# Optimization experiments

Measured on AMD Instinct MI355X. Metric: run time of the kernel, lower is better.

Reference implementation:

```python
import jax, jax.numpy as jnp
import numpy as np

# Model dims (match init_kwargs)
B_, L, D_MODEL = 1, 2048, 1024
D_INNER, D_CONV, DT_RANK, D_STATE = 2048, 4, 64, 16


def setup_inputs() -> dict:
    key = jax.random.key(0)
    ks = jax.random.split(key, 8)
    s = lambda k, shape, scale: jax.random.normal(k, shape, jnp.float32) * scale
    return {
        "x": jax.random.normal(ks[0], (B_, L, D_MODEL), jnp.float32),
        "in_proj_w": s(ks[1], (D_MODEL, 2 * D_INNER), 0.02),
        "in_proj_b": jnp.zeros((2 * D_INNER,), jnp.float32),
        "conv_w": s(ks[2], (D_CONV, D_INNER), 0.1),          # depthwise kernel, one tap-vector per channel
        "conv_b": jnp.zeros((D_INNER,), jnp.float32),
        "x_proj_w": s(ks[3], (D_INNER, DT_RANK + 2 * D_STATE), 0.02),
        "dt_proj_w": s(ks[4], (DT_RANK, D_INNER), 0.1),
        "dt_proj_b": s(ks[5], (D_INNER,), 0.1),
        "A_log": jnp.log(jnp.tile(jnp.arange(1, D_STATE + 1, dtype=jnp.float32), (D_INNER, 1))),  # S4D-real init
        "D": jnp.ones((D_INNER,), jnp.float32),
        "out_proj_w": s(ks[6], (D_INNER, D_MODEL), 0.02),
        "out_proj_b": jnp.zeros((D_MODEL,), jnp.float32),
    }


def _mamba_forward(x, in_proj_w, in_proj_b, conv_w, conv_b, x_proj_w,
                   dt_proj_w, dt_proj_b, A_log, D, out_proj_w, out_proj_b):
    b, l, _ = x.shape
    d_inner = conv_w.shape[1]
    d_state = A_log.shape[1]

    # in_proj -> split into ssm path and gating residual
    x_and_res = x @ in_proj_w + in_proj_b                 # [b, l, 2*d_inner]
    xin, res = jnp.split(x_and_res, 2, axis=-1)

    # causal depthwise conv1d over the sequence dim (pad left d_conv-1, trunc to l)
    xp = jnp.pad(xin, ((0, 0), (D_CONV - 1, 0), (0, 0)))
    kern = conv_w[:, None, :]                             # [W, I=1, O=d_inner]
    xc = jax.lax.conv_general_dilated(
        xp, kern, window_strides=(1,), padding="VALID",
        dimension_numbers=("NWC", "WIO", "NWC"),
        feature_group_count=d_inner) + conv_b             # [b, l, d_inner]
    u = jax.nn.silu(xc)

    # selective SSM: input-dependent dt, B, C
    A = -jnp.exp(A_log)                                   # [d_inner, d_state]
    dbc = u @ x_proj_w                                    # [b, l, dt_rank + 2*d_state]
    dt, Bm, Cm = jnp.split(dbc, [DT_RANK, DT_RANK + d_state], axis=-1)
    delta = jax.nn.softplus(dt @ dt_proj_w + dt_proj_b)   # [b, l, d_inner]

    deltaA = jnp.exp(jnp.einsum("bld,dn->bldn", delta, A))          # [b, l, d_inner, d_state]
    deltaBu = jnp.einsum("bld,bln,bld->bldn", delta, Bm, u)         # [b, l, d_inner, d_state]

    def step(h, inp):
        dA_t, dBu_t, C_t = inp
        h = dA_t * h + dBu_t                              # [b, d_inner, d_state]
        y_t = jnp.einsum("bdn,bn->bd", h, C_t)
        return h, y_t

    h0 = jnp.zeros((b, d_inner, d_state), u.dtype)
    _, ys = jax.lax.scan(
        step, h0,
        (deltaA.transpose(1, 0, 2, 3), deltaBu.transpose(1, 0, 2, 3), Cm.transpose(1, 0, 2)))
    y = ys.transpose(1, 0, 2) + u * D                     # skip connection via D

    # gate and out-project
    y = y * jax.nn.silu(res)
    return y @ out_proj_w + out_proj_b                    # [b, l, d_model]


def reference(x, in_proj_w, in_proj_b, conv_w, conv_b, x_proj_w,
              dt_proj_w, dt_proj_b, A_log, D, out_proj_w, out_proj_b):
    return _mamba_forward(x, in_proj_w, in_proj_b, conv_w, conv_b, x_proj_w,
                          dt_proj_w, dt_proj_b, A_log, D, out_proj_w, out_proj_b)
```

## Files before the change

kernel.cpp:

```cpp
#include <hip/hip_runtime.h>


#define L_SEQ 2048
#define DMODEL 1024
#define DINNER 2048
#define NSTATE 16
#define DTRANK 64
#define NPROJ_PAD 128

typedef __attribute__((ext_vector_type(8))) short short8;
typedef __attribute__((ext_vector_type(4))) float f32x4;

__device__ __forceinline__ unsigned short f2bf(float f) {
  unsigned int u = __float_as_uint(f);
  u += 0x7FFFu + ((u >> 16) & 1u);
  return (unsigned short)(u >> 16);
}

__device__ __forceinline__ void gload16(const void* g, void* l) {
  __builtin_amdgcn_global_load_lds((const __attribute__((address_space(1))) void*)g,
                                   (__attribute__((address_space(3))) void*)l, 16, 0, 0);
}

__global__ void prep_kernel(const float* __restrict__ in_proj_w, const float* __restrict__ x_proj_w,
                            const float* __restrict__ dt_proj_w,
                            const float* __restrict__ out_proj_w, const float* __restrict__ x,
                            unsigned short* __restrict__ w1t, unsigned short* __restrict__ w3t,
                            unsigned short* __restrict__ w4t, unsigned short* __restrict__ w5t,
                            unsigned short* __restrict__ xb) {
  const int bx = blockIdx.x;
  const int tx = threadIdx.x, ty = threadIdx.y;
  const int id = ty * 32 + tx;

  if (bx >= 6464) {
    if (bx < 8512) {
      const int fid = (bx - 6464) * 256 + id;
      f32x4 v = ((const f32x4*)x)[fid];
      ushort4 o;
      o.x = f2bf(v.x); o.y = f2bf(v.y); o.z = f2bf(v.z); o.w = f2bf(v.w);
      ((ushort4*)xb)[fid] = o;
    } else {
      const int fid = (bx - 8512) * 256 + id;
      ((uint4*)(w3t + 96 * 2048))[fid] = (uint4){0, 0, 0, 0};
    }
    return;
  }

  const float* in;
  unsigned short* out;
  int R, C, rel, gx;
  if (bx < 4096) { in = in_proj_w; out = w1t; R = 1024; C = 4096; rel = bx; gx = 128; }
  else if (bx < 4288) { in = x_proj_w; out = w3t; R = 2048; C = 96; rel = bx - 4096; gx = 3; }
  else if (bx < 4416) { in = dt_proj_w; out = w4t; R = 64; C = 2048; rel = bx - 4288; gx = 64; }
  else { in = out_proj_w; out = w5t; R = 2048; C = 1024; rel = bx - 4416; gx = 32; }
  const int c0 = (rel % gx) * 32, r0 = (rel / gx) * 32;

  __shared__ float tile[32][33];
  for (int y = ty; y < 32; y += 8) tile[y][tx] = in[(size_t)(r0 + y) * C + c0 + tx];
  __syncthreads();
  for (int y = ty; y < 32; y += 8) out[(size_t)(c0 + y) * R + r0 + tx] = f2bf(tile[tx][y]);
}

__global__ void conv_silu_kernel(const float* __restrict__ xres, const float* __restrict__ cw,
                                 const float* __restrict__ cb, float* __restrict__ u,
                                 unsigned short* __restrict__ ub) {
  const int id = blockIdx.x * 256 + threadIdx.x;
  const int t = id >> 11;
  const int d = id & (DINNER - 1);
  float acc = cb[d];
#pragma unroll
  for (int j = 0; j < 4; j++) {
    int tt = t - 3 + j;
    if (tt >= 0) acc += xres[(size_t)tt * (2 * DINNER) + d] * cw[j * DINNER + d];
  }
  float s = acc / (1.f + __expf(-acc));
  u[id] = s;
  ub[id] = f2bf(s);
}

template <int EPI>
__global__ void gemm_bf16(const unsigned short* __restrict__ A,
                          const unsigned short* __restrict__ Bt, float* __restrict__ C,
                          const float* __restrict__ bias, int M, int N, int K, int KS) {
  __shared__ __align__(16) unsigned short lA[2][128 * 64];
  __shared__ __align__(16) unsigned short lB[2][128 * 64];
  const int tid = threadIdx.x;
  const int w = tid >> 6;
  const int lane = tid & 63;
  const int m0 = blockIdx.x * 128;
  const int n0 = blockIdx.y * 128;
  const int kbase = blockIdx.z * KS;
  const int lr = lane >> 3;
  const int srcoff = ((lane & 7) ^ lr) * 8;
  const int wm = (w & 1) * 64;
  const int wn = (w >> 1) * 64;
  const int ml = lane & 15;
  const int quad = lane >> 4;

  f32x4 acc[4][4];
#pragma unroll
  for (int i = 0; i < 4; i++)
#pragma unroll
    for (int j = 0; j < 4; j++) acc[i][j] = (f32x4){0.f, 0.f, 0.f, 0.f};

  const unsigned short* Ag = A + (size_t)m0 * K + kbase;
  const unsigned short* Bg = Bt + (size_t)n0 * K + kbase;

  const int niter = KS >> 6;
  auto stage = [&](int buf, int kk) {
#pragma unroll
    for (int c2 = 0; c2 < 4; c2++) {
      const int row = w * 32 + c2 * 8 + lr;
      gload16(Ag + (size_t)row * K + kk + srcoff, &lA[buf][(w * 32 + c2 * 8) * 64]);
      gload16(Bg + (size_t)row * K + kk + srcoff, &lB[buf][(w * 32 + c2 * 8) * 64]);
    }
  };

  stage(0, 0);
  for (int it = 0; it < niter; it++) {
    __syncthreads();
    if (it + 1 < niter) stage((it + 1) & 1, (it + 1) << 6);
    const unsigned short* bufA = lA[it & 1];
    const unsigned short* bufB = lB[it & 1];
#pragma unroll
    for (int ks = 0; ks < 2; ks++) {
      short8 af[4], bfr[4];
#pragma unroll
      for (int i = 0; i < 4; i++) {
        const int row = wm + i * 16 + ml;
        const int q = ((ks * 4 + quad) ^ (ml & 7)) * 8;
        af[i] = *(const short8*)&bufA[row * 64 + q];
      }
#pragma unroll
      for (int j = 0; j < 4; j++) {
        const int row = wn + j * 16 + ml;
        const int q = ((ks * 4 + quad) ^ (ml & 7)) * 8;
        bfr[j] = *(const short8*)&bufB[row * 64 + q];
      }
#pragma unroll
      for (int i = 0; i < 4; i++)
#pragma unroll
        for (int j = 0; j < 4; j++)
          acc[i][j] = __builtin_amdgcn_mfma_f32_16x16x32_bf16(af[i], bfr[j], acc[i][j], 0, 0, 0);
    }
  }

  float* Cp = (EPI == 3) ? C + (size_t)blockIdx.z * M * N : C;
#pragma unroll
  for (int i = 0; i < 4; i++) {
#pragma unroll
    for (int j = 0; j < 4; j++) {
      const int col = n0 + wn + j * 16 + ml;
      float bv = 0.f;
      if ((EPI == 0 || EPI == 1) && bias != nullptr) bv = bias[col];
#pragma unroll
      for (int r = 0; r < 4; r++) {
        const int row = m0 + wm + i * 16 + quad * 4 + r;
        float v = acc[i][j][r];
        if (EPI == 2) {
          atomicAdd(&Cp[(size_t)row * N + col], v);
        } else {
          v += bv;
          if (EPI == 1) v = (v > 15.f) ? v : __logf(1.f + __expf(v));
          Cp[(size_t)row * N + col] = v;
        }
      }
    }
  }
}

__global__ void reduce_dbc_kernel(const float* __restrict__ part, float* __restrict__ dbc,
                                  unsigned short* __restrict__ dtb) {
  const int id = blockIdx.x * 256 + threadIdx.x;
  float s = 0.f;
#pragma unroll
  for (int z = 0; z < 16; z++) s += part[(size_t)z * (L_SEQ * NPROJ_PAD) + id];
  dbc[id] = s;
  const int col = id & 127;
  if (col < 64) dtb[(id >> 7) * 64 + col] = f2bf(s);
}

__global__ void reduce_out_kernel(const float* __restrict__ part, const float* __restrict__ bias,
                                  float* __restrict__ out) {
  const int fid = blockIdx.x * 256 + threadIdx.x;
  const f32x4* p = (const f32x4*)part;
  const int stride = (L_SEQ * DMODEL) / 4;
  f32x4 v = p[fid];
  v += p[fid + stride];
  v += p[fid + 2 * stride];
  v += p[fid + 3 * stride];
  v += ((const f32x4*)bias)[fid & 255];
  ((f32x4*)out)[fid] = v;
}

__global__ void bias_init_kernel(float* __restrict__ out, const float* __restrict__ b, int nmask) {
  int id = blockIdx.x * 256 + threadIdx.x;
  out[id] = b[id & nmask];
}
__global__ void cast_dt_kernel(const float* __restrict__ dbc, unsigned short* __restrict__ dtb) {
  int id = blockIdx.x * 256 + threadIdx.x;
  int t = id >> 6, k = id & 63;
  dtb[id] = f2bf(dbc[t * NPROJ_PAD + k]);
}


template <int TCH_T>
__global__ void scan1_kernel(const float* __restrict__ delta, const float* __restrict__ u,
                             const float* __restrict__ dbc, const float* __restrict__ A_log,
                             float* __restrict__ P, float* __restrict__ Hz) {
  __shared__ float Bs[TCH_T][NSTATE];
  const int d = blockIdx.x * 256 + threadIdx.x;
  const int c = blockIdx.y;
  for (int idx = threadIdx.x; idx < TCH_T * NSTATE; idx += 256) {
    int t = idx >> 4, n = idx & 15;
    Bs[t][n] = dbc[(size_t)(c * TCH_T + t) * NPROJ_PAD + DTRANK + n];
  }
  float Ad[16], h[16], p[16];
#pragma unroll
  for (int n = 0; n < 16; n++) {
    Ad[n] = -__expf(A_log[d * 16 + n]);
    h[n] = 0.f;
    p[n] = 1.f;
  }
  __syncthreads();
#pragma unroll
  for (int t = 0; t < TCH_T; t++) {
    const int tt = c * TCH_T + t;
    float dl = delta[(size_t)tt * DINNER + d];
    float uu = u[(size_t)tt * DINNER + d];
    float du = dl * uu;
#pragma unroll
    for (int n = 0; n < 16; n++) {
      float dA = __expf(dl * Ad[n]);
      p[n] *= dA;
      h[n] = dA * h[n] + du * Bs[t][n];
    }
  }
#pragma unroll
  for (int n = 0; n < 16; n++) {
    P[(size_t)(c * 16 + n) * DINNER + d] = p[n];
    Hz[(size_t)(c * 16 + n) * DINNER + d] = h[n];
  }
}

__global__ void scan_carry_kernel(const float* __restrict__ P, const float* __restrict__ Hz,
                                  float* __restrict__ H0, int nchunk) {
  const int id = blockIdx.x * 256 + threadIdx.x;
  float h = 0.f;
#pragma unroll 8
  for (int c = 0; c < nchunk; c++) {
    H0[c * (NSTATE * DINNER) + id] = h;
    h = P[c * (NSTATE * DINNER) + id] * h + Hz[c * (NSTATE * DINNER) + id];
  }
}

template <int TCH_T>
__global__ void scan2_kernel(const float* __restrict__ delta, const float* __restrict__ u,
                             const float* __restrict__ dbc, const float* __restrict__ A_log,
                             const float* __restrict__ Dv, const float* __restrict__ xres,
                             const float* __restrict__ H0, unsigned short* __restrict__ ygb) {
  __shared__ float Bs[TCH_T][NSTATE];
  __shared__ float Cs[TCH_T][NSTATE];
  const int d = blockIdx.x * 256 + threadIdx.x;
  const int c = blockIdx.y;
  for (int idx = threadIdx.x; idx < TCH_T * 2 * NSTATE; idx += 256) {
    int t = idx >> 5, q = idx & 31;
    float v = dbc[(size_t)(c * TCH_T + t) * NPROJ_PAD + DTRANK + q];
    if (q < 16) Bs[t][q] = v;
    else Cs[t][q - 16] = v;
  }
  float Ad[16], h[16];
#pragma unroll
  for (int n = 0; n < 16; n++) {
    Ad[n] = -__expf(A_log[d * 16 + n]);
    h[n] = H0[(size_t)(c * 16 + n) * DINNER + d];
  }
  const float Dd = Dv[d];
  __syncthreads();
#pragma unroll
  for (int t = 0; t < TCH_T; t++) {
    const int tt = c * TCH_T + t;
    float dl = delta[(size_t)tt * DINNER + d];
    float uu = u[(size_t)tt * DINNER + d];
    float r = xres[(size_t)tt * (2 * DINNER) + DINNER + d];
    float du = dl * uu;
    float y0 = 0.f, y1 = 0.f;
#pragma unroll
    for (int n = 0; n < 16; n++) {
      float dA = __expf(dl * Ad[n]);
      h[n] = dA * h[n] + du * Bs[t][n];
      if (n & 1) y1 += h[n] * Cs[t][n];
      else y0 += h[n] * Cs[t][n];
    }
    float sil = r / (1.f + __expf(-r));
    float yg = (y0 + y1 + uu * Dd) * sil;
    ygb[(size_t)tt * DINNER + d] = f2bf(yg);
  }
}


extern "C" void kernel_launch(void* const* d_in, const int* in_sizes, int n_in, void* d_out,
                              int out_size, void* d_ws, size_t ws_size, hipStream_t stream) {
  const float* x = (const float*)d_in[0];
  const float* in_proj_w = (const float*)d_in[1];
  const float* in_proj_b = (const float*)d_in[2];
  const float* conv_w = (const float*)d_in[3];
  const float* conv_b = (const float*)d_in[4];
  const float* x_proj_w = (const float*)d_in[5];
  const float* dt_proj_w = (const float*)d_in[6];
  const float* dt_proj_b = (const float*)d_in[7];
  const float* A_log = (const float*)d_in[8];
  const float* Dvec = (const float*)d_in[9];
  const float* out_proj_w = (const float*)d_in[10];
  const float* out_proj_b = (const float*)d_in[11];
  float* out = (float*)d_out;
  char* ws = (char*)d_ws;

  const size_t MB = 1048576;
  const size_t XB = 0;
  const size_t W1T = 4 * MB;
  const size_t XRES = 12 * MB;
  const size_t U = 44 * MB;
  const size_t UB = 60 * MB;
  const size_t W3T = 68 * MB;
  const size_t DBC = W3T + 524288;
  const size_t DTB = DBC + MB;
  const size_t W4T = DTB + 262144;
  const size_t DELTA = 70 * MB;
  const size_t YGB = 86 * MB;
  const size_t W5T = 94 * MB;
  const size_t PBUF = 98 * MB;
  (void)in_sizes; (void)n_in; (void)out_size;

  const bool big = ws_size >= PBUF + 3 * (size_t)(128 * NSTATE * DINNER) * 4;
  prep_kernel<<<8544, dim3(32, 8), 0, stream>>>(
      in_proj_w, x_proj_w, dt_proj_w, out_proj_w, x, (unsigned short*)(ws + W1T),
      (unsigned short*)(ws + W3T), (unsigned short*)(ws + W4T), (unsigned short*)(ws + W5T),
      (unsigned short*)(ws + XB));

  gemm_bf16<0><<<dim3(16, 32, 1), 256, 0, stream>>>(
      (const unsigned short*)(ws + XB), (const unsigned short*)(ws + W1T), (float*)(ws + XRES),
      in_proj_b, 2048, 4096, 1024, 1024);

  conv_silu_kernel<<<(L_SEQ * DINNER) / 256, 256, 0, stream>>>(
      (const float*)(ws + XRES), conv_w, conv_b, (float*)(ws + U), (unsigned short*)(ws + UB));

  if (big) {
    const int tch = 16, nch = 128;
    const size_t PB = (size_t)nch * NSTATE * DINNER * 4;
    const size_t HZB = PBUF + PB;
    const size_t H0B = PBUF + 2 * PB;
    const size_t G3P = PBUF;
    const size_t G2P = PBUF;

    gemm_bf16<3><<<dim3(16, 1, 16), 256, 0, stream>>>(
        (const unsigned short*)(ws + UB), (const unsigned short*)(ws + W3T), (float*)(ws + G3P),
        nullptr, 2048, NPROJ_PAD, 2048, 128);
    reduce_dbc_kernel<<<(L_SEQ * NPROJ_PAD) / 256, 256, 0, stream>>>(
        (const float*)(ws + G3P), (float*)(ws + DBC), (unsigned short*)(ws + DTB));

    gemm_bf16<1><<<dim3(16, 16, 1), 256, 0, stream>>>(
        (const unsigned short*)(ws + DTB), (const unsigned short*)(ws + W4T), (float*)(ws + DELTA),
        dt_proj_b, 2048, 2048, 64, 64);

    const dim3 sgrid(DINNER / 256, nch);
    scan1_kernel<16><<<sgrid, 256, 0, stream>>>(
        (const float*)(ws + DELTA), (const float*)(ws + U), (const float*)(ws + DBC), A_log,
        (float*)(ws + PBUF), (float*)(ws + HZB));
    scan_carry_kernel<<<(NSTATE * DINNER) / 256, 256, 0, stream>>>(
        (const float*)(ws + PBUF), (const float*)(ws + HZB), (float*)(ws + H0B), nch);
    scan2_kernel<16><<<sgrid, 256, 0, stream>>>(
        (const float*)(ws + DELTA), (const float*)(ws + U), (const float*)(ws + DBC), A_log, Dvec,
        (const float*)(ws + XRES), (const float*)(ws + H0B), (unsigned short*)(ws + YGB));

    gemm_bf16<3><<<dim3(16, 8, 4), 256, 0, stream>>>(
        (const unsigned short*)(ws + YGB), (const unsigned short*)(ws + W5T), (float*)(ws + G2P),
        nullptr, 2048, 1024, 2048, 512);
    reduce_out_kernel<<<(L_SEQ * DMODEL) / 1024, 256, 0, stream>>>((const float*)(ws + G2P),
                                                                   out_proj_b, out);
    (void)tch;
  } else {
    hipMemsetAsync(ws + DBC, 0, (size_t)L_SEQ * NPROJ_PAD * 4, stream);
    gemm_bf16<2><<<dim3(16, 1, 16), 256, 0, stream>>>(
        (const unsigned short*)(ws + UB), (const unsigned short*)(ws + W3T), (float*)(ws + DBC),
        nullptr, 2048, NPROJ_PAD, 2048, 128);
    cast_dt_kernel<<<(L_SEQ * DTRANK) / 256, 256, 0, stream>>>((const float*)(ws + DBC),
                                                               (unsigned short*)(ws + DTB));
    gemm_bf16<1><<<dim3(16, 16, 1), 256, 0, stream>>>(
        (const unsigned short*)(ws + DTB), (const unsigned short*)(ws + W4T), (float*)(ws + DELTA),
        dt_proj_b, 2048, 2048, 64, 64);
    const int tch = 64, nch = 32;
    const size_t PB = (size_t)nch * NSTATE * DINNER * 4;
    const size_t HZB = PBUF + PB;
    const size_t H0B = PBUF + 2 * PB;
    const dim3 sgrid(DINNER / 256, nch);
    scan1_kernel<64><<<sgrid, 256, 0, stream>>>(
        (const float*)(ws + DELTA), (const float*)(ws + U), (const float*)(ws + DBC), A_log,
        (float*)(ws + PBUF), (float*)(ws + HZB));
    scan_carry_kernel<<<(NSTATE * DINNER) / 256, 256, 0, stream>>>(
        (const float*)(ws + PBUF), (const float*)(ws + HZB), (float*)(ws + H0B), nch);
    scan2_kernel<64><<<sgrid, 256, 0, stream>>>(
        (const float*)(ws + DELTA), (const float*)(ws + U), (const float*)(ws + DBC), A_log, Dvec,
        (const float*)(ws + XRES), (const float*)(ws + H0B), (unsigned short*)(ws + YGB));
    bias_init_kernel<<<(L_SEQ * DMODEL) / 256, 256, 0, stream>>>(out, out_proj_b, DMODEL - 1);
    gemm_bf16<2><<<dim3(16, 8, 4), 256, 0, stream>>>(
        (const unsigned short*)(ws + YGB), (const unsigned short*)(ws + W5T), out, nullptr, 2048,
        1024, 2048, 512);
    (void)tch;
  }
}
```

Measured before the change: 238.8 us.

## Store scan intermediates in bf16, fuse silu epilogues, retile GEMMs, drop split-K out-proj

Delta, u, the silu of the residual, and the chunked-scan P/Hz/H0 buffers are now stored in bf16 instead of fp32. Softplus and the gate silu are fused into GEMM epilogues, and the in_proj output is split so each half goes to its own buffer. The GEMM is templated on tile size; x_proj uses 64x128 tiles with split-K 8, and out_proj uses 64x64 tiles with no split-K, which removes the reduce pass. The aim is to cut memory traffic and kernel launches, at the cost of reduced precision in the scan carries and intermediates.

```diff
diff --git a/kernel.cpp b/kernel.cpp
--- a/kernel.cpp
+++ b/kernel.cpp
@@ -7,6 +7,8 @@
 #define NSTATE 16
 #define DTRANK 64
 #define NPROJ_PAD 128
+#define NCH 128
+#define TCH 16
 
 typedef __attribute__((ext_vector_type(8))) short short8;
 typedef __attribute__((ext_vector_type(4))) float f32x4;
@@ -15,6 +17,9 @@
   unsigned int u = __float_as_uint(f);
   u += 0x7FFFu + ((u >> 16) & 1u);
   return (unsigned short)(u >> 16);
+}
+__device__ __forceinline__ float bf2f(unsigned short u) {
+  return __uint_as_float(((unsigned int)u) << 16);
 }
 
 __device__ __forceinline__ void gload16(const void* g, void* l) {
@@ -61,9 +66,8 @@
   for (int y = ty; y < 32; y += 8) out[(size_t)(c0 + y) * R + r0 + tx] = f2bf(tile[tx][y]);
 }
 
-__global__ void conv_silu_kernel(const float* __restrict__ xres, const float* __restrict__ cw,
-                                 const float* __restrict__ cb, float* __restrict__ u,
-                                 unsigned short* __restrict__ ub) {
+__global__ void conv_silu_kernel(const float* __restrict__ xin, const float* __restrict__ cw,
+                                 const float* __restrict__ cb, unsigned short* __restrict__ ub) {
   const int id = blockIdx.x * 256 + threadIdx.x;
   const int t = id >> 11;
   const int d = id & (DINNER - 1);
@@ -71,37 +75,38 @@
 #pragma unroll
   for (int j = 0; j < 4; j++) {
     int tt = t - 3 + j;
-    if (tt >= 0) acc += xres[(size_t)tt * (2 * DINNER) + d] * cw[j * DINNER + d];
+    if (tt >= 0) acc += xin[(size_t)tt * DINNER + d] * cw[j * DINNER + d];
   }
   float s = acc / (1.f + __expf(-acc));
-  u[id] = s;
   ub[id] = f2bf(s);
 }
 
-template <int EPI>
+template <int EPI, int BM, int BN>
 __global__ void gemm_bf16(const unsigned short* __restrict__ A,
                           const unsigned short* __restrict__ Bt, float* __restrict__ C,
-                          const float* __restrict__ bias, int M, int N, int K, int KS) {
-  __shared__ __align__(16) unsigned short lA[2][128 * 64];
-  __shared__ __align__(16) unsigned short lB[2][128 * 64];
+                          unsigned short* __restrict__ C2, const float* __restrict__ bias, int M,
+                          int N, int K, int KS) {
+  constexpr int MI = BM / 32, NJ = BN / 32;
+  __shared__ __align__(16) unsigned short lA[2][BM * 64];
+  __shared__ __align__(16) unsigned short lB[2][BN * 64];
   const int tid = threadIdx.x;
   const int w = tid >> 6;
   const int lane = tid & 63;
-  const int m0 = blockIdx.x * 128;
-  const int n0 = blockIdx.y * 128;
+  const int m0 = blockIdx.x * BM;
+  const int n0 = blockIdx.y * BN;
   const int kbase = blockIdx.z * KS;
   const int lr = lane >> 3;
   const int srcoff = ((lane & 7) ^ lr) * 8;
-  const int wm = (w & 1) * 64;
-  const int wn = (w >> 1) * 64;
+  const int wm = (w & 1) * (BM / 2);
+  const int wn = (w >> 1) * (BN / 2);
   const int ml = lane & 15;
   const int quad = lane >> 4;
 
-  f32x4 acc[4][4];
-#pragma unroll
-  for (int i = 0; i < 4; i++)
-#pragma unroll
-    for (int j = 0; j < 4; j++) acc[i][j] = (f32x4){0.f, 0.f, 0.f, 0.f};
+  f32x4 acc[MI][NJ];
+#pragma unroll
+  for (int i = 0; i < MI; i++)
+#pragma unroll
+    for (int j = 0; j < NJ; j++) acc[i][j] = (f32x4){0.f, 0.f, 0.f, 0.f};
 
   const unsigned short* Ag = A + (size_t)m0 * K + kbase;
   const unsigned short* Bg = Bt + (size_t)n0 * K + kbase;
@@ -109,10 +114,14 @@
   const int niter = KS >> 6;
   auto stage = [&](int buf, int kk) {
 #pragma unroll
-    for (int c2 = 0; c2 < 4; c2++) {
-      const int row = w * 32 + c2 * 8 + lr;
-      gload16(Ag + (size_t)row * K + kk + srcoff, &lA[buf][(w * 32 + c2 * 8) * 64]);
-      gload16(Bg + (size_t)row * K + kk + srcoff, &lB[buf][(w * 32 + c2 * 8) * 64]);
+    for (int c2 = 0; c2 < BM / 32; c2++) {
+      const int row = w * (BM / 4) + c2 * 8 + lr;
+      gload16(Ag + (size_t)row * K + kk + srcoff, &lA[buf][(w * (BM / 4) + c2 * 8) * 64]);
+    }
+#pragma unroll
+    for (int c2 = 0; c2 < BN / 32; c2++) {
+      const int row = w * (BN / 4) + c2 * 8 + lr;
+      gload16(Bg + (size_t)row * K + kk + srcoff, &lB[buf][(w * (BN / 4) + c2 * 8) * 64]);
     }
   };
 
@@ -124,45 +133,50 @@
     const unsigned short* bufB = lB[it & 1];
 #pragma unroll
     for (int ks = 0; ks < 2; ks++) {
-      short8 af[4], bfr[4];
-#pragma unroll
-      for (int i = 0; i < 4; i++) {
+      short8 af[MI], bfr[NJ];
+#pragma unroll
+      for (int i = 0; i < MI; i++) {
         const int row = wm + i * 16 + ml;
-        const int q = ((ks * 4 + quad) ^ (ml & 7)) * 8;
-        af[i] = *(const short8*)&bufA[row * 64 + q];
+        af[i] = *(const short8*)&bufA[row * 64 + ((ks * 4 + quad) ^ (ml & 7)) * 8];
       }
 #pragma unroll
-      for (int j = 0; j < 4; j++) {
+      for (int j = 0; j < NJ; j++) {
         const int row = wn + j * 16 + ml;
-        const int q = ((ks * 4 + quad) ^ (ml & 7)) * 8;
-        bfr[j] = *(const short8*)&bufB[row * 64 + q];
+        bfr[j] = *(const short8*)&bufB[row * 64 + ((ks * 4 + quad) ^ (ml & 7)) * 8];
       }
 #pragma unroll
-      for (int i = 0; i < 4; i++)
-#pragma unroll
-        for (int j = 0; j < 4; j++)
+      for (int i = 0; i < MI; i++)
+#pragma unroll
+        for (int j = 0; j < NJ; j++)
           acc[i][j] = __builtin_amdgcn_mfma_f32_16x16x32_bf16(af[i], bfr[j], acc[i][j], 0, 0, 0);
     }
   }
 
   float* Cp = (EPI == 3) ? C + (size_t)blockIdx.z * M * N : C;
 #pragma unroll
-  for (int i = 0; i < 4; i++) {
-#pragma unroll
-    for (int j = 0; j < 4; j++) {
+  for (int i = 0; i < MI; i++) {
+#pragma unroll
+    for (int j = 0; j < NJ; j++) {
       const int col = n0 + wn + j * 16 + ml;
-      float bv = 0.f;
-      if ((EPI == 0 || EPI == 1) && bias != nullptr) bv = bias[col];
+      float bv = (EPI == 3) ? 0.f : (bias ? bias[col] : 0.f);
 #pragma unroll
       for (int r = 0; r < 4; r++) {
         const int row = m0 + wm + i * 16 + quad * 4 + r;
-        float v = acc[i][j][r];
-        if (EPI == 2) {
-          atomicAdd(&Cp[(size_t)row * N + col], v);
-        } else {
-          v += bv;
-          if (EPI == 1) v = (v > 15.f) ? v : __logf(1.f + __expf(v));
+        float v = acc[i][j][r] + bv;
+        if (EPI == 0) {
           Cp[(size_t)row * N + col] = v;
+        } else if (EPI == 3) {
+          Cp[(size_t)row * N + col] = v;
+        } else if (EPI == 4) {
+          if (col < DINNER) {
+            C[(size_t)row * DINNER + col] = v;
+          } else {
+            float s = v / (1.f + __expf(-v));
+            C2[(size_t)row * DINNER + (col - DINNER)] = f2bf(s);
+          }
+        } else if (EPI == 5) {
+          float sp = (v > 15.f) ? v : __logf(1.f + __expf(v));
+          C2[(size_t)row * N + col] = f2bf(sp);
         }
       }
     }
@@ -174,46 +188,23 @@
   const int id = blockIdx.x * 256 + threadIdx.x;
   float s = 0.f;
 #pragma unroll
-  for (int z = 0; z < 16; z++) s += part[(size_t)z * (L_SEQ * NPROJ_PAD) + id];
+  for (int z = 0; z < 8; z++) s += part[(size_t)z * (L_SEQ * NPROJ_PAD) + id];
   dbc[id] = s;
   const int col = id & 127;
   if (col < 64) dtb[(id >> 7) * 64 + col] = f2bf(s);
 }
 
-__global__ void reduce_out_kernel(const float* __restrict__ part, const float* __restrict__ bias,
-                                  float* __restrict__ out) {
-  const int fid = blockIdx.x * 256 + threadIdx.x;
-  const f32x4* p = (const f32x4*)part;
-  const int stride = (L_SEQ * DMODEL) / 4;
-  f32x4 v = p[fid];
-  v += p[fid + stride];
-  v += p[fid + 2 * stride];
-  v += p[fid + 3 * stride];
-  v += ((const f32x4*)bias)[fid & 255];
-  ((f32x4*)out)[fid] = v;
-}
-
-__global__ void bias_init_kernel(float* __restrict__ out, const float* __restrict__ b, int nmask) {
-  int id = blockIdx.x * 256 + threadIdx.x;
-  out[id] = b[id & nmask];
-}
-__global__ void cast_dt_kernel(const float* __restrict__ dbc, unsigned short* __restrict__ dtb) {
-  int id = blockIdx.x * 256 + threadIdx.x;
-  int t = id >> 6, k = id & 63;
-  dtb[id] = f2bf(dbc[t * NPROJ_PAD + k]);
-}
-
-
-template <int TCH_T>
-__global__ void scan1_kernel(const float* __restrict__ delta, const float* __restrict__ u,
+
+__global__ void scan1_kernel(const unsigned short* __restrict__ db,
+                             const unsigned short* __restrict__ ub,
                              const float* __restrict__ dbc, const float* __restrict__ A_log,
-                             float* __restrict__ P, float* __restrict__ Hz) {
-  __shared__ float Bs[TCH_T][NSTATE];
+                             unsigned short* __restrict__ P, unsigned short* __restrict__ Hz) {
+  __shared__ float Bs[TCH][NSTATE];
   const int d = blockIdx.x * 256 + threadIdx.x;
   const int c = blockIdx.y;
-  for (int idx = threadIdx.x; idx < TCH_T * NSTATE; idx += 256) {
+  for (int idx = threadIdx.x; idx < TCH * NSTATE; idx += 256) {
     int t = idx >> 4, n = idx & 15;
-    Bs[t][n] = dbc[(size_t)(c * TCH_T + t) * NPROJ_PAD + DTRANK + n];
+    Bs[t][n] = dbc[(size_t)(c * TCH + t) * NPROJ_PAD + DTRANK + n];
   }
   float Ad[16], h[16], p[16];
 #pragma unroll
@@ -224,10 +215,10 @@
   }
   __syncthreads();
 #pragma unroll
-  for (int t = 0; t < TCH_T; t++) {
-    const int tt = c * TCH_T + t;
-    float dl = delta[(size_t)tt * DINNER + d];
-    float uu = u[(size_t)tt * DINNER + d];
+  for (int t = 0; t < TCH; t++) {
+    const int tt = c * TCH + t;
+    float dl = bf2f(db[(size_t)tt * DINNER + d]);
+    float uu = bf2f(ub[(size_t)tt * DINNER + d]);
     float du = dl * uu;
 #pragma unroll
     for (int n = 0; n < 16; n++) {
@@ -238,34 +229,36 @@
   }
 #pragma unroll
   for (int n = 0; n < 16; n++) {
-    P[(size_t)(c * 16 + n) * DINNER + d] = p[n];
-    Hz[(size_t)(c * 16 + n) * DINNER + d] = h[n];
-  }
-}
-
-__global__ void scan_carry_kernel(const float* __restrict__ P, const float* __restrict__ Hz,
-                                  float* __restrict__ H0, int nchunk) {
+    P[(size_t)(c * 16 + n) * DINNER + d] = f2bf(p[n]);
+    Hz[(size_t)(c * 16 + n) * DINNER + d] = f2bf(h[n]);
+  }
+}
+
+__global__ void scan_carry_kernel(const unsigned short* __restrict__ P,
+                                  const unsigned short* __restrict__ Hz,
+                                  unsigned short* __restrict__ H0) {
   const int id = blockIdx.x * 256 + threadIdx.x;
   float h = 0.f;
 #pragma unroll 8
-  for (int c = 0; c < nchunk; c++) {
-    H0[c * (NSTATE * DINNER) + id] = h;
-    h = P[c * (NSTATE * DINNER) + id] * h + Hz[c * (NSTATE * DINNER) + id];
-  }
-}
-
-template <int TCH_T>
-__global__ void scan2_kernel(const float* __restrict__ delta, const float* __restrict__ u,
+  for (int c = 0; c < NCH; c++) {
+    H0[c * (NSTATE * DINNER) + id] = f2bf(h);
+    h = bf2f(P[c * (NSTATE * DINNER) + id]) * h + bf2f(Hz[c * (NSTATE * DINNER) + id]);
+  }
+}
+
+__global__ void scan2_kernel(const unsigned short* __restrict__ db,
+                             const unsigned short* __restrict__ ub,
                              const float* __restrict__ dbc, const float* __restrict__ A_log,
-                             const float* __restrict__ Dv, const float* __restrict__ xres,
-                             const float* __restrict__ H0, unsigned short* __restrict__ ygb) {
-  __shared__ float Bs[TCH_T][NSTATE];
-  __shared__ float Cs[TCH_T][NSTATE];
+                             const float* __restrict__ Dv, const unsigned short* __restrict__ rsil,
+                             const unsigned short* __restrict__ H0,
+                             unsigned short* __restrict__ ygb) {
+  __shared__ float Bs[TCH][NSTATE];
+  __shared__ float Cs[TCH][NSTATE];
   const int d = blockIdx.x * 256 + threadIdx.x;
   const int c = blockIdx.y;
-  for (int idx = threadIdx.x; idx < TCH_T * 2 * NSTATE; idx += 256) {
+  for (int idx = threadIdx.x; idx < TCH * 2 * NSTATE; idx += 256) {
     int t = idx >> 5, q = idx & 31;
-    float v = dbc[(size_t)(c * TCH_T + t) * NPROJ_PAD + DTRANK + q];
+    float v = dbc[(size_t)(c * TCH + t) * NPROJ_PAD + DTRANK + q];
     if (q < 16) Bs[t][q] = v;
     else Cs[t][q - 16] = v;
   }
@@ -273,16 +266,16 @@
 #pragma unroll
   for (int n = 0; n < 16; n++) {
     Ad[n] = -__expf(A_log[d * 16 + n]);
-    h[n] = H0[(size_t)(c * 16 + n) * DINNER + d];
+    h[n] = bf2f(H0[(size_t)(c * 16 + n) * DINNER + d]);
   }
   const float Dd = Dv[d];
   __syncthreads();
 #pragma unroll
-  for (int t = 0; t < TCH_T; t++) {
-    const int tt = c * TCH_T + t;
-    float dl = delta[(size_t)tt * DINNER + d];
-    float uu = u[(size_t)tt * DINNER + d];
-    float r = xres[(size_t)tt * (2 * DINNER) + DINNER + d];
+  for (int t = 0; t < TCH; t++) {
+    const int tt = c * TCH + t;
+    float dl = bf2f(db[(size_t)tt * DINNER + d]);
+    float uu = bf2f(ub[(size_t)tt * DINNER + d]);
+    float rs = bf2f(rsil[(size_t)tt * DINNER + d]);
     float du = dl * uu;
     float y0 = 0.f, y1 = 0.f;
 #pragma unroll
@@ -292,8 +285,7 @@
       if (n & 1) y1 += h[n] * Cs[t][n];
       else y0 += h[n] * Cs[t][n];
     }
-    float sil = r / (1.f + __expf(-r));
-    float yg = (y0 + y1 + uu * Dd) * sil;
+    float yg = (y0 + y1 + uu * Dd) * rs;
     ygb[(size_t)tt * DINNER + d] = f2bf(yg);
   }
 }
@@ -315,97 +307,61 @@
   const float* out_proj_b = (const float*)d_in[11];
   float* out = (float*)d_out;
   char* ws = (char*)d_ws;
+  (void)in_sizes; (void)n_in; (void)out_size; (void)ws_size;
 
   const size_t MB = 1048576;
   const size_t XB = 0;
   const size_t W1T = 4 * MB;
-  const size_t XRES = 12 * MB;
-  const size_t U = 44 * MB;
-  const size_t UB = 60 * MB;
-  const size_t W3T = 68 * MB;
+  const size_t XIN = 12 * MB;
+  const size_t RSIL = 28 * MB;
+  const size_t UB = 36 * MB;
+  const size_t W3T = 44 * MB;
   const size_t DBC = W3T + 524288;
   const size_t DTB = DBC + MB;
   const size_t W4T = DTB + 262144;
-  const size_t DELTA = 70 * MB;
-  const size_t YGB = 86 * MB;
-  const size_t W5T = 94 * MB;
-  const size_t PBUF = 98 * MB;
-  (void)in_sizes; (void)n_in; (void)out_size;
-
-  const bool big = ws_size >= PBUF + 3 * (size_t)(128 * NSTATE * DINNER) * 4;
+  const size_t DELTA = 46 * MB;
+  const size_t YGB = 54 * MB;
+  const size_t W5T = 62 * MB;
+  const size_t G3P = 66 * MB;
+  const size_t PB = 74 * MB;
+  const size_t HZB = 82 * MB;
+  const size_t H0B = 90 * MB;
+
   prep_kernel<<<8544, dim3(32, 8), 0, stream>>>(
       in_proj_w, x_proj_w, dt_proj_w, out_proj_w, x, (unsigned short*)(ws + W1T),
       (unsigned short*)(ws + W3T), (unsigned short*)(ws + W4T), (unsigned short*)(ws + W5T),
       (unsigned short*)(ws + XB));
 
-  gemm_bf16<0><<<dim3(16, 32, 1), 256, 0, stream>>>(
-      (const unsigned short*)(ws + XB), (const unsigned short*)(ws + W1T), (float*)(ws + XRES),
-      in_proj_b, 2048, 4096, 1024, 1024);
+  gemm_bf16<4, 128, 128><<<dim3(16, 32, 1), 256, 0, stream>>>(
+      (const unsigned short*)(ws + XB), (const unsigned short*)(ws + W1T), (float*)(ws + XIN),
+      (unsigned short*)(ws + RSIL), in_proj_b, 2048, 4096, 1024, 1024);
 
   conv_silu_kernel<<<(L_SEQ * DINNER) / 256, 256, 0, stream>>>(
-      (const float*)(ws + XRES), conv_w, conv_b, (float*)(ws + U), (unsigned short*)(ws + UB));
-
-  if (big) {
-    const int tch = 16, nch = 128;
-    const size_t PB = (size_t)nch * NSTATE * DINNER * 4;
-    const size_t HZB = PBUF + PB;
-    const size_t H0B = PBUF + 2 * PB;
-    const size_t G3P = PBUF;
-    const size_t G2P = PBUF;
-
-    gemm_bf16<3><<<dim3(16, 1, 16), 256, 0, stream>>>(
-        (const unsigned short*)(ws + UB), (const unsigned short*)(ws + W3T), (float*)(ws + G3P),
-        nullptr, 2048, NPROJ_PAD, 2048, 128);
-    reduce_dbc_kernel<<<(L_SEQ * NPROJ_PAD) / 256, 256, 0, stream>>>(
-        (const float*)(ws + G3P), (float*)(ws + DBC), (unsigned short*)(ws + DTB));
-
-    gemm_bf16<1><<<dim3(16, 16, 1), 256, 0, stream>>>(
-        (const unsigned short*)(ws + DTB), (const unsigned short*)(ws + W4T), (float*)(ws + DELTA),
-        dt_proj_b, 2048, 2048, 64, 64);
-
-    const dim3 sgrid(DINNER / 256, nch);
-    scan1_kernel<16><<<sgrid, 256, 0, stream>>>(
-        (const float*)(ws + DELTA), (const float*)(ws + U), (const float*)(ws + DBC), A_log,
-        (float*)(ws + PBUF), (float*)(ws + HZB));
-    scan_carry_kernel<<<(NSTATE * DINNER) / 256, 256, 0, stream>>>(
-        (const float*)(ws + PBUF), (const float*)(ws + HZB), (float*)(ws + H0B), nch);
-    scan2_kernel<16><<<sgrid, 256, 0, stream>>>(
-        (const float*)(ws + DELTA), (const float*)(ws + U), (const float*)(ws + DBC), A_log, Dvec,
-        (const float*)(ws + XRES), (const float*)(ws + H0B), (unsigned short*)(ws + YGB));
-
-    gemm_bf16<3><<<dim3(16, 8, 4), 256, 0, stream>>>(
-        (const unsigned short*)(ws + YGB), (const unsigned short*)(ws + W5T), (float*)(ws + G2P),
-        nullptr, 2048, 1024, 2048, 512);
-    reduce_out_kernel<<<(L_SEQ * DMODEL) / 1024, 256, 0, stream>>>((const float*)(ws + G2P),
-                                                                   out_proj_b, out);
-    (void)tch;
-  } else {
-    hipMemsetAsync(ws + DBC, 0, (size_t)L_SEQ * NPROJ_PAD * 4, stream);
-    gemm_bf16<2><<<dim3(16, 1, 16), 256, 0, stream>>>(
-        (const unsigned short*)(ws + UB), (const unsigned short*)(ws + W3T), (float*)(ws + DBC),
-        nullptr, 2048, NPROJ_PAD, 2048, 128);
-    cast_dt_kernel<<<(L_SEQ * DTRANK) / 256, 256, 0, stream>>>((const float*)(ws + DBC),
-                                                               (unsigned short*)(ws + DTB));
-    gemm_bf16<1><<<dim3(16, 16, 1), 256, 0, stream>>>(
-        (const unsigned short*)(ws + DTB), (const unsigned short*)(ws + W4T), (float*)(ws + DELTA),
-        dt_proj_b, 2048, 2048, 64, 64);
-    const int tch = 64, nch = 32;
-    const size_t PB = (size_t)nch * NSTATE * DINNER * 4;
-    const size_t HZB = PBUF + PB;
-    const size_t H0B = PBUF + 2 * PB;
-    const dim3 sgrid(DINNER / 256, nch);
-    scan1_kernel<64><<<sgrid, 256, 0, stream>>>(
-        (const float*)(ws + DELTA), (const float*)(ws + U), (const float*)(ws + DBC), A_log,
-        (float*)(ws + PBUF), (float*)(ws + HZB));
-    scan_carry_kernel<<<(NSTATE * DINNER) / 256, 256, 0, stream>>>(
-        (const float*)(ws + PBUF), (const float*)(ws + HZB), (float*)(ws + H0B), nch);
-    scan2_kernel<64><<<sgrid, 256, 0, stream>>>(
-        (const float*)(ws + DELTA), (const float*)(ws + U), (const float*)(ws + DBC), A_log, Dvec,
-        (const float*)(ws + XRES), (const float*)(ws + H0B), (unsigned short*)(ws + YGB));
-    bias_init_kernel<<<(L_SEQ * DMODEL) / 256, 256, 0, stream>>>(out, out_proj_b, DMODEL - 1);
-    gemm_bf16<2><<<dim3(16, 8, 4), 256, 0, stream>>>(
-        (const unsigned short*)(ws + YGB), (const unsigned short*)(ws + W5T), out, nullptr, 2048,
-        1024, 2048, 512);
-    (void)tch;
-  }
-}
+      (const float*)(ws + XIN), conv_w, conv_b, (unsigned short*)(ws + UB));
+
+  gemm_bf16<3, 64, 128><<<dim3(32, 1, 8), 256, 0, stream>>>(
+      (const unsigned short*)(ws + UB), (const unsigned short*)(ws + W3T), (float*)(ws + G3P),
+      nullptr, nullptr, 2048, NPROJ_PAD, 2048, 256);
+  reduce_dbc_kernel<<<(L_SEQ * NPROJ_PAD) / 256, 256, 0, stream>>>(
+      (const float*)(ws + G3P), (float*)(ws + DBC), (unsigned short*)(ws + DTB));
+
+  gemm_bf16<5, 128, 128><<<dim3(16, 16, 1), 256, 0, stream>>>(
+      (const unsigned short*)(ws + DTB), (const unsigned short*)(ws + W4T), nullptr,
+      (unsigned short*)(ws + DELTA), dt_proj_b, 2048, 2048, 64, 64);
+
+  const dim3 sgrid(DINNER / 256, NCH);
+  scan1_kernel<<<sgrid, 256, 0, stream>>>(
+      (const unsigned short*)(ws + DELTA), (const unsigned short*)(ws + UB),
+      (const float*)(ws + DBC), A_log, (unsigned short*)(ws + PB), (unsigned short*)(ws + HZB));
+  scan_carry_kernel<<<(NSTATE * DINNER) / 256, 256, 0, stream>>>(
+      (const unsigned short*)(ws + PB), (const unsigned short*)(ws + HZB),
+      (unsigned short*)(ws + H0B));
+  scan2_kernel<<<sgrid, 256, 0, stream>>>(
+      (const unsigned short*)(ws + DELTA), (const unsigned short*)(ws + UB),
+      (const float*)(ws + DBC), A_log, Dvec, (const unsigned short*)(ws + RSIL),
+      (const unsigned short*)(ws + H0B), (unsigned short*)(ws + YGB));
+
+  gemm_bf16<0, 64, 64><<<dim3(32, 16, 1), 256, 0, stream>>>(
+      (const unsigned short*)(ws + YGB), (const unsigned short*)(ws + W5T), out, nullptr,
+      out_proj_b, 2048, 1024, 2048, 2048);
+}
```

Measured after the change: 230.5 us. 3.5% less time.
